# Kernel optimization log

Measured on AMD Instinct MI355X. Metric: run time of the kernel, lower is better.

## Reference

```python
import jax, jax.numpy as jnp
import numpy as np

IN_FEATURES = 4096
OUT_FEATURES = 11008
BATCH = 16


def setup_inputs() -> dict:
    key = jax.random.key(0)
    k1, k2, k3 = jax.random.split(key, 3)
    x = jax.random.normal(k1, (BATCH, IN_FEATURES), dtype=jnp.float32)
    # int8 quantized weight codes, stored as int32 in [0,255] then shifted to [-128,127]
    w_q = jax.random.randint(k2, (OUT_FEATURES, IN_FEATURES), 0, 255, dtype=jnp.int32)
    # per-tensor quantization scale (max(|w|)/127 in the original; any positive scalar here)
    scale = jnp.ones((1,), dtype=jnp.float32) * 0.01
    bias = jax.random.normal(k3, (OUT_FEATURES,), dtype=jnp.float32)
    return {"x": x, "w_q": w_q, "scale": scale, "bias": bias}


def reference(x, w_q, scale, bias):
    # Codec decode is lossless on the int8 codes; math-relevant part is
    # dequantize (codes * scale) followed by F.linear(x, W, b).
    codes = w_q.astype(jnp.float32) - 128.0  # shift to signed int8 range
    weight = codes * scale[0]                 # [out_features, in_features]
    return x @ weight.T + bias                # [batch, out_features]
```

## Files before the change

kernel.cpp:

```cpp
#include <hip/hip_runtime.h>
#include <stdint.h>


constexpr int IN_F  = 4096;
constexpr int OUT_F = 11008;
constexpr int NWAVES = 8;
constexpr int KB_PER_WAVE = IN_F / 32 / NWAVES;

typedef _Float16 f16x8 __attribute__((ext_vector_type(8)));
typedef float    f32x4 __attribute__((ext_vector_type(4)));

__global__ __launch_bounds__(NWAVES * 64, 1)
void qlinear_mfma(const float* __restrict__ x,
                  const int*   __restrict__ wq,
                  const float* __restrict__ scale,
                  const float* __restrict__ bias,
                  float*       __restrict__ out)
{
    const int tid  = threadIdx.x;
    const int lane = tid & 63;
    const int wave = tid >> 6;
    const int obase = blockIdx.x * 16;

    const int ncol = lane & 15;
    const int kgrp = lane >> 4;

    const int o  = obase + ncol;
    const int k0 = wave * (KB_PER_WAVE * 32) + kgrp * 8;

    const float* xp = x  + (size_t)ncol * IN_F + k0;
    const int*   wp = wq + (size_t)o    * IN_F + k0;

    f32x4 acc = {0.f, 0.f, 0.f, 0.f};

    #pragma unroll 4
    for (int it = 0; it < KB_PER_WAVE; ++it) {
        const float4 xa = *reinterpret_cast<const float4*>(xp);
        const float4 xb = *reinterpret_cast<const float4*>(xp + 4);
        const int4   wa = *reinterpret_cast<const int4*>(wp);
        const int4   wb = *reinterpret_cast<const int4*>(wp + 4);

        f16x8 af, bf;
        af[0] = (_Float16)xa.x; af[1] = (_Float16)xa.y;
        af[2] = (_Float16)xa.z; af[3] = (_Float16)xa.w;
        af[4] = (_Float16)xb.x; af[5] = (_Float16)xb.y;
        af[6] = (_Float16)xb.z; af[7] = (_Float16)xb.w;

        bf[0] = (_Float16)(wa.x - 128); bf[1] = (_Float16)(wa.y - 128);
        bf[2] = (_Float16)(wa.z - 128); bf[3] = (_Float16)(wa.w - 128);
        bf[4] = (_Float16)(wb.x - 128); bf[5] = (_Float16)(wb.y - 128);
        bf[6] = (_Float16)(wb.z - 128); bf[7] = (_Float16)(wb.w - 128);

        acc = __builtin_amdgcn_mfma_f32_16x16x32_f16(af, bf, acc, 0, 0, 0);

        xp += 32;
        wp += 32;
    }

    __shared__ f32x4 red[NWAVES][64];
    red[wave][lane] = acc;
    __syncthreads();

    if (wave == 0) {
        f32x4 s = red[0][lane];
        #pragma unroll
        for (int w = 1; w < NWAVES; ++w) s += red[w][lane];

        const float sc = scale[0];
        const float bo = bias[o];
        const int   brow = kgrp * 4;
        #pragma unroll
        for (int r = 0; r < 4; ++r)
            out[(size_t)(brow + r) * OUT_F + o] = s[r] * sc + bo;
    }
}

extern "C" void kernel_launch(void* const* d_in, const int* in_sizes, int n_in,
                              void* d_out, int out_size, void* d_ws, size_t ws_size,
                              hipStream_t stream) {
    const float* x     = (const float*)d_in[0];
    const int*   wq    = (const int*)d_in[1];
    const float* scale = (const float*)d_in[2];
    const float* bias  = (const float*)d_in[3];
    float*       out   = (float*)d_out;

    dim3 grid(OUT_F / 16);
    dim3 block(NWAVES * 64);
    qlinear_mfma<<<grid, block, 0, stream>>>(x, wq, scale, bias, out);
}
```

Baseline: 49.15 us.

## Preload x fragments into registers and double-buffer weight loads across MFMA groups

```diff
diff --git a/kernel.cpp b/kernel.cpp
--- a/kernel.cpp
+++ b/kernel.cpp
@@ -5,10 +5,26 @@
 constexpr int IN_F  = 4096;
 constexpr int OUT_F = 11008;
 constexpr int NWAVES = 8;
-constexpr int KB_PER_WAVE = IN_F / 32 / NWAVES;
+constexpr int KPW = IN_F / NWAVES;
+constexpr int NKB = KPW / 32;
+constexpr int GRP = 4;
+constexpr int NGRP = NKB / GRP;
 
 typedef _Float16 f16x8 __attribute__((ext_vector_type(8)));
 typedef float    f32x4 __attribute__((ext_vector_type(4)));
+
+__device__ inline f16x8 cvt_codes(int4 a, int4 b) {
+    f16x8 r;
+    r[0] = (_Float16)(short)(a.x - 128);
+    r[1] = (_Float16)(short)(a.y - 128);
+    r[2] = (_Float16)(short)(a.z - 128);
+    r[3] = (_Float16)(short)(a.w - 128);
+    r[4] = (_Float16)(short)(b.x - 128);
+    r[5] = (_Float16)(short)(b.y - 128);
+    r[6] = (_Float16)(short)(b.z - 128);
+    r[7] = (_Float16)(short)(b.w - 128);
+    return r;
+}
 
 __global__ __launch_bounds__(NWAVES * 64, 1)
 void qlinear_mfma(const float* __restrict__ x,
@@ -26,35 +42,51 @@
     const int kgrp = lane >> 4;
 
     const int o  = obase + ncol;
-    const int k0 = wave * (KB_PER_WAVE * 32) + kgrp * 8;
+    const int k0 = wave * KPW + kgrp * 8;
 
-    const float* xp = x  + (size_t)ncol * IN_F + k0;
-    const int*   wp = wq + (size_t)o    * IN_F + k0;
+    const float* xp = x + (size_t)ncol * IN_F + k0;
+    f16x8 a[NKB];
+    #pragma unroll
+    for (int kb = 0; kb < NKB; ++kb) {
+        const float4 xa = *reinterpret_cast<const float4*>(xp + kb * 32);
+        const float4 xb = *reinterpret_cast<const float4*>(xp + kb * 32 + 4);
+        f16x8 t;
+        t[0] = (_Float16)xa.x; t[1] = (_Float16)xa.y;
+        t[2] = (_Float16)xa.z; t[3] = (_Float16)xa.w;
+        t[4] = (_Float16)xb.x; t[5] = (_Float16)xb.y;
+        t[6] = (_Float16)xb.z; t[7] = (_Float16)xb.w;
+        a[kb] = t;
+    }
+
+    const int* wp = wq + (size_t)o * IN_F + k0;
+
+    int4 cur[2 * GRP], nxt[2 * GRP];
+    #pragma unroll
+    for (int i = 0; i < GRP; ++i) {
+        cur[2 * i]     = *reinterpret_cast<const int4*>(wp + i * 32);
+        cur[2 * i + 1] = *reinterpret_cast<const int4*>(wp + i * 32 + 4);
+    }
 
     f32x4 acc = {0.f, 0.f, 0.f, 0.f};
 
-    #pragma unroll 4
-    for (int it = 0; it < KB_PER_WAVE; ++it) {
-        const float4 xa = *reinterpret_cast<const float4*>(xp);
-        const float4 xb = *reinterpret_cast<const float4*>(xp + 4);
-        const int4   wa = *reinterpret_cast<const int4*>(wp);
-        const int4   wb = *reinterpret_cast<const int4*>(wp + 4);
-
-        f16x8 af, bf;
-        af[0] = (_Float16)xa.x; af[1] = (_Float16)xa.y;
-        af[2] = (_Float16)xa.z; af[3] = (_Float16)xa.w;
-        af[4] = (_Float16)xb.x; af[5] = (_Float16)xb.y;
-        af[6] = (_Float16)xb.z; af[7] = (_Float16)xb.w;
-
-        bf[0] = (_Float16)(wa.x - 128); bf[1] = (_Float16)(wa.y - 128);
-        bf[2] = (_Float16)(wa.z - 128); bf[3] = (_Float16)(wa.w - 128);
-        bf[4] = (_Float16)(wb.x - 128); bf[5] = (_Float16)(wb.y - 128);
-        bf[6] = (_Float16)(wb.z - 128); bf[7] = (_Float16)(wb.w - 128);
-
-        acc = __builtin_amdgcn_mfma_f32_16x16x32_f16(af, bf, acc, 0, 0, 0);
-
-        xp += 32;
-        wp += 32;
+    #pragma unroll
+    for (int g = 0; g < NGRP; ++g) {
+        if (g < NGRP - 1) {
+            #pragma unroll
+            for (int i = 0; i < GRP; ++i) {
+                nxt[2 * i]     = *reinterpret_cast<const int4*>(wp + ((g + 1) * GRP + i) * 32);
+                nxt[2 * i + 1] = *reinterpret_cast<const int4*>(wp + ((g + 1) * GRP + i) * 32 + 4);
+            }
+        }
+        #pragma unroll
+        for (int i = 0; i < GRP; ++i) {
+            const f16x8 bf = cvt_codes(cur[2 * i], cur[2 * i + 1]);
+            acc = __builtin_amdgcn_mfma_f32_16x16x32_f16(a[g * GRP + i], bf, acc, 0, 0, 0);
+        }
+        if (g < NGRP - 1) {
+            #pragma unroll
+            for (int i = 0; i < 2 * GRP; ++i) cur[i] = nxt[i];
+        }
     }
 
     __shared__ f32x4 red[NWAVES][64];
```

Result: no change. 49.10 us (-0.1%).

## Stage weight tiles into LDS via async global_load_lds with double buffering

Applied to the files above, without the earlier changes.

```diff
diff --git a/kernel.cpp b/kernel.cpp
--- a/kernel.cpp
+++ b/kernel.cpp
@@ -5,18 +5,33 @@
 constexpr int IN_F  = 4096;
 constexpr int OUT_F = 11008;
 constexpr int NWAVES = 8;
-constexpr int KB_PER_WAVE = IN_F / 32 / NWAVES;
+constexpr int BK = 512;
+constexpr int NCHUNK = IN_F / BK;
+constexpr int ROW_BYTES = BK * 4;
+constexpr int CHUNK_BYTES = 16 * ROW_BYTES;
 
 typedef _Float16 f16x8 __attribute__((ext_vector_type(8)));
 typedef float    f32x4 __attribute__((ext_vector_type(4)));
 
-__global__ __launch_bounds__(NWAVES * 64, 1)
+__device__ inline f16x8 cvt_codes(int4 a, int4 b) {
+    f16x8 r;
+    r[0] = (_Float16)(a.x - 128); r[1] = (_Float16)(a.y - 128);
+    r[2] = (_Float16)(a.z - 128); r[3] = (_Float16)(a.w - 128);
+    r[4] = (_Float16)(b.x - 128); r[5] = (_Float16)(b.y - 128);
+    r[6] = (_Float16)(b.z - 128); r[7] = (_Float16)(b.w - 128);
+    return r;
+}
+
+__global__ __launch_bounds__(NWAVES * 64, 4)
 void qlinear_mfma(const float* __restrict__ x,
                   const int*   __restrict__ wq,
                   const float* __restrict__ scale,
                   const float* __restrict__ bias,
                   float*       __restrict__ out)
 {
+    __shared__ __align__(16) char smem[2 * CHUNK_BYTES];
+    __shared__ f32x4 red[NWAVES][64];
+
     const int tid  = threadIdx.x;
     const int lane = tid & 63;
     const int wave = tid >> 6;
@@ -25,39 +40,62 @@
     const int ncol = lane & 15;
     const int kgrp = lane >> 4;
 
-    const int o  = obase + ncol;
-    const int k0 = wave * (KB_PER_WAVE * 32) + kgrp * 8;
+    f16x8 a[2 * NCHUNK];
+    {
+        const float* xp = x + (size_t)ncol * IN_F;
+        #pragma unroll
+        for (int f = 0; f < 2 * NCHUNK; ++f) {
+            const int c  = f >> 1, jj = f & 1;
+            const int kb = c * BK + (wave * 2 + jj) * 32 + kgrp * 8;
+            const float4 xa = *reinterpret_cast<const float4*>(xp + kb);
+            const float4 xb = *reinterpret_cast<const float4*>(xp + kb + 4);
+            f16x8 t;
+            t[0] = (_Float16)xa.x; t[1] = (_Float16)xa.y;
+            t[2] = (_Float16)xa.z; t[3] = (_Float16)xa.w;
+            t[4] = (_Float16)xb.x; t[5] = (_Float16)xb.y;
+            t[6] = (_Float16)xb.z; t[7] = (_Float16)xb.w;
+            a[f] = t;
+        }
+    }
 
-    const float* xp = x  + (size_t)ncol * IN_F + k0;
-    const int*   wp = wq + (size_t)o    * IN_F + k0;
+    const char* wq_bytes = reinterpret_cast<const char*>(wq);
+    auto stage = [&](int c, int buf) {
+        #pragma unroll
+        for (int p = 0; p < 4; ++p) {
+            const int row = p * 4 + (wave >> 1);
+            const int within = (((wave & 1) * 1024) + lane * 16) ^ ((row & 7) << 4);
+            const char* src = wq_bytes + (size_t)(obase + row) * (IN_F * 4)
+                                       + (size_t)c * ROW_BYTES + within;
+            char* dst = smem + buf * CHUNK_BYTES + p * 8192 + wave * 1024 + lane * 16;
+            __builtin_amdgcn_global_load_lds(
+                (const __attribute__((address_space(1))) void*)src,
+                (__attribute__((address_space(3))) void*)dst, 16, 0, 0);
+        }
+    };
+
+    stage(0, 0);
+    __syncthreads();
 
     f32x4 acc = {0.f, 0.f, 0.f, 0.f};
+    const int swz = (ncol & 7) << 4;
 
-    #pragma unroll 4
-    for (int it = 0; it < KB_PER_WAVE; ++it) {
-        const float4 xa = *reinterpret_cast<const float4*>(xp);
-        const float4 xb = *reinterpret_cast<const float4*>(xp + 4);
-        const int4   wa = *reinterpret_cast<const int4*>(wp);
-        const int4   wb = *reinterpret_cast<const int4*>(wp + 4);
+    for (int c = 0; c < NCHUNK; ++c) {
+        const int buf = c & 1;
+        if (c + 1 < NCHUNK) stage(c + 1, buf ^ 1);
 
-        f16x8 af, bf;
-        af[0] = (_Float16)xa.x; af[1] = (_Float16)xa.y;
-        af[2] = (_Float16)xa.z; af[3] = (_Float16)xa.w;
-        af[4] = (_Float16)xb.x; af[5] = (_Float16)xb.y;
-        af[6] = (_Float16)xb.z; af[7] = (_Float16)xb.w;
-
-        bf[0] = (_Float16)(wa.x - 128); bf[1] = (_Float16)(wa.y - 128);
-        bf[2] = (_Float16)(wa.z - 128); bf[3] = (_Float16)(wa.w - 128);
-        bf[4] = (_Float16)(wb.x - 128); bf[5] = (_Float16)(wb.y - 128);
-        bf[6] = (_Float16)(wb.z - 128); bf[7] = (_Float16)(wb.w - 128);
-
-        acc = __builtin_amdgcn_mfma_f32_16x16x32_f16(af, bf, acc, 0, 0, 0);
-
-        xp += 32;
-        wp += 32;
+        const char* rowbase = smem + buf * CHUNK_BYTES + ncol * ROW_BYTES;
+        #pragma unroll
+        for (int jj = 0; jj < 2; ++jj) {
+            const int kb = wave * 2 + jj;
+            const int lo = kgrp * 32 + kb * 128;
+            const int4 w0 = *reinterpret_cast<const int4*>(rowbase + ((lo)      ^ swz));
+            const int4 w1 = *reinterpret_cast<const int4*>(rowbase + ((lo + 16) ^ swz));
+            const f16x8 bf = cvt_codes(w0, w1);
+            acc = __builtin_amdgcn_mfma_f32_16x16x32_f16(a[c * 2 + jj], bf, acc, 0, 0, 0);
+        }
+        __syncthreads();
     }
 
-    __shared__ f32x4 red[NWAVES][64];
     red[wave][lane] = acc;
     __syncthreads();
 
@@ -67,11 +105,11 @@
         for (int w = 1; w < NWAVES; ++w) s += red[w][lane];
 
         const float sc = scale[0];
-        const float bo = bias[o];
+        const float bo = bias[obase + ncol];
         const int   brow = kgrp * 4;
         #pragma unroll
         for (int r = 0; r < 4; ++r)
-            out[(size_t)(brow + r) * OUT_F + o] = s[r] * sc + bo;
+            out[(size_t)(brow + r) * OUT_F + obase + ncol] = s[r] * sc + bo;
     }
 }
 
```

Measured after the change: 55.17 us. 1.12x slower.

## Stagger K slices per block, fully unroll loop, use nontemporal weight loads

Applied to the files above, without the earlier changes.

```diff
diff --git a/kernel.cpp b/kernel.cpp
--- a/kernel.cpp
+++ b/kernel.cpp
@@ -5,12 +5,14 @@
 constexpr int IN_F  = 4096;
 constexpr int OUT_F = 11008;
 constexpr int NWAVES = 8;
-constexpr int KB_PER_WAVE = IN_F / 32 / NWAVES;
+constexpr int KPW = IN_F / NWAVES;
+constexpr int NKB = KPW / 32;
 
 typedef _Float16 f16x8 __attribute__((ext_vector_type(8)));
 typedef float    f32x4 __attribute__((ext_vector_type(4)));
+typedef int      i32x4 __attribute__((ext_vector_type(4)));
 
-__global__ __launch_bounds__(NWAVES * 64, 1)
+__global__ __launch_bounds__(NWAVES * 64)
 void qlinear_mfma(const float* __restrict__ x,
                   const int*   __restrict__ wq,
                   const float* __restrict__ scale,
@@ -25,36 +27,38 @@
     const int ncol = lane & 15;
     const int kgrp = lane >> 4;
 
-    const int o  = obase + ncol;
-    const int k0 = wave * (KB_PER_WAVE * 32) + kgrp * 8;
+    const int o = obase + ncol;
+
+    const int kslice = (wave + (int)blockIdx.x) & (NWAVES - 1);
+    const int k0 = kslice * KPW + kgrp * 8;
 
     const float* xp = x  + (size_t)ncol * IN_F + k0;
     const int*   wp = wq + (size_t)o    * IN_F + k0;
 
     f32x4 acc = {0.f, 0.f, 0.f, 0.f};
 
-    #pragma unroll 4
-    for (int it = 0; it < KB_PER_WAVE; ++it) {
-        const float4 xa = *reinterpret_cast<const float4*>(xp);
-        const float4 xb = *reinterpret_cast<const float4*>(xp + 4);
-        const int4   wa = *reinterpret_cast<const int4*>(wp);
-        const int4   wb = *reinterpret_cast<const int4*>(wp + 4);
+    #pragma unroll
+    for (int kb = 0; kb < NKB; ++kb) {
+        const int off = kb * 32;
+        const f32x4 xa = *reinterpret_cast<const f32x4*>(xp + off);
+        const f32x4 xb = *reinterpret_cast<const f32x4*>(xp + off + 4);
+        const i32x4 wa = __builtin_nontemporal_load(
+            reinterpret_cast<const i32x4*>(wp + off));
+        const i32x4 wb = __builtin_nontemporal_load(
+            reinterpret_cast<const i32x4*>(wp + off + 4));
 
         f16x8 af, bf;
-        af[0] = (_Float16)xa.x; af[1] = (_Float16)xa.y;
-        af[2] = (_Float16)xa.z; af[3] = (_Float16)xa.w;
-        af[4] = (_Float16)xb.x; af[5] = (_Float16)xb.y;
-        af[6] = (_Float16)xb.z; af[7] = (_Float16)xb.w;
+        af[0] = (_Float16)xa[0]; af[1] = (_Float16)xa[1];
+        af[2] = (_Float16)xa[2]; af[3] = (_Float16)xa[3];
+        af[4] = (_Float16)xb[0]; af[5] = (_Float16)xb[1];
+        af[6] = (_Float16)xb[2]; af[7] = (_Float16)xb[3];
 
-        bf[0] = (_Float16)(wa.x - 128); bf[1] = (_Float16)(wa.y - 128);
-        bf[2] = (_Float16)(wa.z - 128); bf[3] = (_Float16)(wa.w - 128);
-        bf[4] = (_Float16)(wb.x - 128); bf[5] = (_Float16)(wb.y - 128);
-        bf[6] = (_Float16)(wb.z - 128); bf[7] = (_Float16)(wb.w - 128);
+        bf[0] = (_Float16)(wa[0] - 128); bf[1] = (_Float16)(wa[1] - 128);
+        bf[2] = (_Float16)(wa[2] - 128); bf[3] = (_Float16)(wa[3] - 128);
+        bf[4] = (_Float16)(wb[0] - 128); bf[5] = (_Float16)(wb[1] - 128);
+        bf[6] = (_Float16)(wb[2] - 128); bf[7] = (_Float16)(wb[3] - 128);
 
         acc = __builtin_amdgcn_mfma_f32_16x16x32_f16(af, bf, acc, 0, 0, 0);
-
-        xp += 32;
-        wp += 32;
     }
 
     __shared__ f32x4 red[NWAVES][64];
```

Measured after the change: 55.54 us. +13.0%, slower.
